# Kernel optimization log

Hardware: AMD Instinct MI355X
Metric: run time of the kernel (lower is better)

Reference implementation:

```python
import jax, jax.numpy as jnp
import numpy as np
from jax.ops import segment_sum

NUM_NODES = 100000
HIDDEN = 128
NUM_LAYERS = 3
EDGES = 640000
BN_EPS = 1e-5


def setup_inputs() -> dict:
    key = jax.random.key(0)
    ks = jax.random.split(key, 6)
    edge_index = jax.random.randint(ks[0], (2, EDGES), 0, NUM_NODES, dtype=jnp.int32)
    # xavier-ish init for embedding (hidden-1 dims; last dim is log-degree feature)
    emb_weight = jax.random.normal(ks[1], (NUM_NODES, HIDDEN - 1), dtype=jnp.float32) * 0.02
    # GCNConv linear weights [L, in, out] and biases [L, out]
    Ws = jax.random.normal(ks[2], (NUM_LAYERS, HIDDEN, HIDDEN), dtype=jnp.float32) * (1.0 / np.sqrt(HIDDEN))
    bs = jnp.zeros((NUM_LAYERS, HIDDEN), dtype=jnp.float32)
    gammas = jnp.ones((NUM_LAYERS, HIDDEN), dtype=jnp.float32)
    betas = jnp.zeros((NUM_LAYERS, HIDDEN), dtype=jnp.float32)
    return {"emb_weight": emb_weight, "Ws": Ws, "bs": bs,
            "gammas": gammas, "betas": betas, "edge_index": edge_index}


def reference(emb_weight, Ws, bs, gammas, betas, edge_index):
    row, col = edge_index[0], edge_index[1]  # source, target
    N = emb_weight.shape[0]
    ones_e = jnp.ones(row.shape[0], dtype=emb_weight.dtype)

    # node_degree_features = log(out_degree + 1) (degree of edge_index[0])
    deg_src = segment_sum(ones_e, row, num_segments=N)
    x = jnp.concatenate([emb_weight, jnp.log(deg_src + 1.0)[:, None]], axis=1)  # [N, H]

    # GCN symmetric normalization (add_self_loops=False): deg over targets
    deg = segment_sum(ones_e, col, num_segments=N)
    dinv = jnp.where(deg > 0, jax.lax.rsqrt(jnp.maximum(deg, 1.0)), 0.0)
    norm = dinv[row] * dinv[col]  # [E]

    for i in range(Ws.shape[0]):
        x_prev = x
        h = x @ Ws[i]  # [N, H]
        # scatter-add of normalized messages: out[col] += norm * h[row]
        agg = segment_sum(norm[:, None] * h[row], col, num_segments=N) + bs[i]
        # BatchNorm1d (batch statistics, biased variance)
        mean = agg.mean(axis=0)
        var = agg.var(axis=0)
        x = gammas[i] * (agg - mean) * jax.lax.rsqrt(var + BN_EPS) + betas[i]
        x = jax.nn.relu(x)
        if i > 0:
            x = x + 0.5 * x_prev
    return x
```

## Files before the change

kernel.cpp:

```cpp
#include <hip/hip_runtime.h>
#include <hip/hip_bf16.h>
#include <math.h>

#define BN_EPS 1e-5f

typedef __attribute__((ext_vector_type(8))) short short8v;
typedef __attribute__((ext_vector_type(4))) float f32x4;

__device__ inline float bf_lo(unsigned int p) { return __uint_as_float(p << 16); }
__device__ inline float bf_hi(unsigned int p) { return __uint_as_float(p & 0xffff0000u); }
__device__ inline unsigned int packbf(float a, float b) {
    unsigned short lo = __builtin_bit_cast(unsigned short, __float2bfloat16(a));
    unsigned short hi = __builtin_bit_cast(unsigned short, __float2bfloat16(b));
    return (unsigned int)lo | ((unsigned int)hi << 16);
}


__global__ __launch_bounds__(256) void deg_kernel(const int* __restrict__ row, const int* __restrict__ col,
                                                  float* __restrict__ deg_src, float* __restrict__ deg_dst, int E) {
    int e = blockIdx.x * 256 + threadIdx.x;
    if (e < E) {
        atomicAdd(&deg_src[row[e]], 1.0f);
        atomicAdd(&deg_dst[col[e]], 1.0f);
    }
}

__global__ __launch_bounds__(256) void dinv_cnt_kernel(float* __restrict__ deg_dst, int* __restrict__ cnt, int N) {
    int n = blockIdx.x * 256 + threadIdx.x;
    if (n < N) {
        float d = deg_dst[n];
        cnt[n] = (int)d;
        deg_dst[n] = (d > 0.0f) ? rsqrtf(d) : 0.0f;
    }
}

__global__ __launch_bounds__(256) void initx_kernel(const float* __restrict__ emb, const float* __restrict__ deg_src,
                                                    unsigned int* __restrict__ x, int N) {
    int idx = blockIdx.x * 256 + threadIdx.x;
    if (idx < N * 64) {
        int n = idx >> 6, p = idx & 63;
        float v0, v1;
        if (p < 63) {
            v0 = emb[(size_t)n * 127 + 2 * p];
            v1 = emb[(size_t)n * 127 + 2 * p + 1];
        } else {
            v0 = emb[(size_t)n * 127 + 126];
            v1 = logf(deg_src[n] + 1.0f);
        }
        x[idx] = packbf(v0, v1);
    }
}

__global__ __launch_bounds__(256) void wt_kernel(const float* __restrict__ Ws, __hip_bfloat16* __restrict__ Wt) {
    int idx = blockIdx.x * 256 + threadIdx.x;
    if (idx < 3 * 16384) {
        int l = idx >> 14, rem = idx & 16383, c = rem >> 7, k = rem & 127;
        Wt[idx] = __float2bfloat16(Ws[(l << 14) + (k << 7) + c]);
    }
}


__global__ __launch_bounds__(256) void scan_pass1(const int* __restrict__ cnt, int* __restrict__ blockSums,
                                                  int N, int PT) {
    __shared__ int lds[256];
    const int tid = threadIdx.x;
    const int start = (blockIdx.x * 256 + tid) * PT;
    int s = 0;
    for (int i = 0; i < PT; ++i) {
        int idx = start + i;
        if (idx < N) s += cnt[idx];
    }
    lds[tid] = s;
    __syncthreads();
    for (int d = 128; d > 0; d >>= 1) {
        if (tid < d) lds[tid] += lds[tid + d];
        __syncthreads();
    }
    if (tid == 0) blockSums[blockIdx.x] = lds[0];
}

__global__ __launch_bounds__(256) void scan_pass2(const int* __restrict__ blockSums, int* __restrict__ blockOffs) {
    __shared__ int lds[256];
    const int tid = threadIdx.x;
    int v = blockSums[tid];
    lds[tid] = v;
    __syncthreads();
    for (int d = 1; d < 256; d <<= 1) {
        int t = (tid >= d) ? lds[tid - d] : 0;
        __syncthreads();
        lds[tid] += t;
        __syncthreads();
    }
    blockOffs[tid] = lds[tid] - v;
}

__global__ __launch_bounds__(256) void scan_pass3(const int* __restrict__ cnt, const int* __restrict__ blockOffs,
                                                  int* __restrict__ off, int* __restrict__ cur,
                                                  int N, int PT, int E) {
    __shared__ int lds[256];
    const int tid = threadIdx.x;
    const int start = (blockIdx.x * 256 + tid) * PT;
    int s = 0;
    for (int i = 0; i < PT; ++i) {
        int idx = start + i;
        if (idx < N) s += cnt[idx];
    }
    lds[tid] = s;
    __syncthreads();
    for (int d = 1; d < 256; d <<= 1) {
        int t = (tid >= d) ? lds[tid - d] : 0;
        __syncthreads();
        lds[tid] += t;
        __syncthreads();
    }
    int prefix = blockOffs[blockIdx.x] + lds[tid] - s;
    for (int i = 0; i < PT; ++i) {
        int idx = start + i;
        if (idx < N) {
            off[idx] = prefix;
            cur[idx] = prefix;
            prefix += cnt[idx];
        }
    }
    if (blockIdx.x == 0 && tid == 0) off[N] = E;
}

__global__ __launch_bounds__(256) void fill_kernel(const int* __restrict__ row, const int* __restrict__ col,
                                                   const float* __restrict__ dinv, int* __restrict__ cur,
                                                   int* __restrict__ srcs, float* __restrict__ wts, int E) {
    int e = blockIdx.x * 256 + threadIdx.x;
    if (e < E) {
        int r = row[e], t = col[e];
        int p = atomicAdd(&cur[t], 1);
        srcs[p] = r;
        wts[p] = dinv[r] * dinv[t];
    }
}


__global__ __launch_bounds__(256) void gemm_mfma(const __hip_bfloat16* __restrict__ X,
                                                 const __hip_bfloat16* __restrict__ Wt,
                                                 __hip_bfloat16* __restrict__ H, int nStripes, int N) {
    const int lane = threadIdx.x & 63;
    const int wv = threadIdx.x >> 6;
    const int r = lane & 15;
    const int q = lane >> 4;
    const int ch = (blockIdx.x * 4 + wv) & 1;

    short8v bfrag[4][4];
#pragma unroll
    for (int ct = 0; ct < 4; ++ct)
#pragma unroll
        for (int kk = 0; kk < 4; ++kk)
            bfrag[ct][kk] = *(const short8v*)(Wt + ((ch * 64 + ct * 16 + r) << 7) + kk * 32 + q * 8);

    const int totalJobs = nStripes * 2;
    for (int job = blockIdx.x * 4 + wv; job < totalJobs; job += gridDim.x * 4) {
        const int s = job >> 1;
        const int arow = s * 16 + r;
        short8v a0 = {}, a1 = {}, a2 = {}, a3 = {};
        if (arow < N) {
            const __hip_bfloat16* xp = X + ((size_t)arow << 7) + q * 8;
            a0 = *(const short8v*)(xp);
            a1 = *(const short8v*)(xp + 32);
            a2 = *(const short8v*)(xp + 64);
            a3 = *(const short8v*)(xp + 96);
        }
        f32x4 acc[4];
#pragma unroll
        for (int ct = 0; ct < 4; ++ct) {
            f32x4 c = {0.f, 0.f, 0.f, 0.f};
            c = __builtin_amdgcn_mfma_f32_16x16x32_bf16(a0, bfrag[ct][0], c, 0, 0, 0);
            c = __builtin_amdgcn_mfma_f32_16x16x32_bf16(a1, bfrag[ct][1], c, 0, 0, 0);
            c = __builtin_amdgcn_mfma_f32_16x16x32_bf16(a2, bfrag[ct][2], c, 0, 0, 0);
            c = __builtin_amdgcn_mfma_f32_16x16x32_bf16(a3, bfrag[ct][3], c, 0, 0, 0);
            acc[ct] = c;
        }
#pragma unroll
        for (int g = 0; g < 4; ++g) {
            int grow = s * 16 + q * 4 + g;
            if (grow < N) {
                __hip_bfloat16* hp = H + ((size_t)grow << 7) + ch * 64 + r;
#pragma unroll
                for (int ct = 0; ct < 4; ++ct)
                    hp[ct * 16] = __float2bfloat16(acc[ct][g]);
            }
        }
    }
}


__global__ __launch_bounds__(256) void gather_kernel(const __hip_bfloat16* __restrict__ h,
                                                     const int* __restrict__ off, const int* __restrict__ srcs,
                                                     const float* __restrict__ wts, const float* __restrict__ bias,
                                                     float* __restrict__ agg, float* __restrict__ sums, int N) {
    __shared__ float sm[2][4][128];
    const int tid = threadIdx.x;
    const int lane = tid & 63;
    const int w = tid >> 6;
    const int g = lane >> 4;
    const int s = lane & 15;

    float b8[8];
    *(float4*)&b8[0] = *(const float4*)&bias[s * 8];
    *(float4*)&b8[4] = *(const float4*)&bias[s * 8 + 4];

    float psum[8], psq[8];
#pragma unroll
    for (int j = 0; j < 8; ++j) { psum[j] = 0.f; psq[j] = 0.f; }

    for (int n0 = blockIdx.x * 4 + w; n0 < N; n0 += gridDim.x * 4) {
        const int n = __builtin_amdgcn_readfirstlane(n0);
        const int sOff = off[n], eOff = off[n + 1];
        float acc[8];
#pragma unroll
        for (int j = 0; j < 8; ++j) acc[j] = 0.f;

        for (int i = sOff; i < eOff; i += 8) {
            int i0 = i + g, i1 = i + 4 + g;
            int idx0 = (i0 < eOff) ? i0 : (eOff - 1);
            int idx1 = (i1 < eOff) ? i1 : (eOff - 1);
            float w0 = (i0 < eOff) ? wts[idx0] : 0.0f;
            float w1 = (i1 < eOff) ? wts[idx1] : 0.0f;
            int r0 = srcs[idx0], r1 = srcs[idx1];
            short8v h0 = *(const short8v*)(h + ((size_t)r0 << 7) + s * 8);
            short8v h1 = *(const short8v*)(h + ((size_t)r1 << 7) + s * 8);
#pragma unroll
            for (int j = 0; j < 4; ++j) {
                unsigned int u0 = ((const unsigned int*)&h0)[j];
                unsigned int u1 = ((const unsigned int*)&h1)[j];
                acc[2 * j]     = fmaf(w0, bf_lo(u0), acc[2 * j]);
                acc[2 * j + 1] = fmaf(w0, bf_hi(u0), acc[2 * j + 1]);
                acc[2 * j]     = fmaf(w1, bf_lo(u1), acc[2 * j]);
                acc[2 * j + 1] = fmaf(w1, bf_hi(u1), acc[2 * j + 1]);
            }
        }
#pragma unroll
        for (int j = 0; j < 8; ++j) {
            acc[j] += __shfl_xor(acc[j], 16);
            acc[j] += __shfl_xor(acc[j], 32);
            acc[j] += b8[j];
        }
        if (g == 0) {
            float* ap = &agg[((size_t)n << 7) + s * 8];
            *(float4*)ap       = make_float4(acc[0], acc[1], acc[2], acc[3]);
            *(float4*)(ap + 4) = make_float4(acc[4], acc[5], acc[6], acc[7]);
#pragma unroll
            for (int j = 0; j < 8; ++j) {
                psum[j] += acc[j];
                psq[j] = fmaf(acc[j], acc[j], psq[j]);
            }
        }
    }
    if (g == 0) {
#pragma unroll
        for (int j = 0; j < 8; ++j) {
            sm[0][w][s * 8 + j] = psum[j];
            sm[1][w][s * 8 + j] = psq[j];
        }
    }
    __syncthreads();
    if (tid < 128) {
        atomicAdd(&sums[tid], sm[0][0][tid] + sm[0][1][tid] + sm[0][2][tid] + sm[0][3][tid]);
    } else {
        int c = tid - 128;
        atomicAdd(&sums[128 + c], sm[1][0][c] + sm[1][1][c] + sm[1][2][c] + sm[1][3][c]);
    }
}


__global__ void bn_finalize(const float* __restrict__ sums, const float* __restrict__ gamma,
                            const float* __restrict__ beta, float* __restrict__ ss, int N) {
    int c = threadIdx.x;
    float mean = sums[c] / (float)N;
    float var  = sums[128 + c] / (float)N - mean * mean;
    float inv  = rsqrtf(fmaxf(var, 0.0f) + BN_EPS);
    float sc   = gamma[c] * inv;
    ss[c]       = sc;
    ss[128 + c] = beta[c] - mean * sc;
}

template <int MODE>
__global__ __launch_bounds__(256) void bn_apply(const float* __restrict__ agg, const float* __restrict__ ss,
                                                const unsigned int* __restrict__ xprev, void* __restrict__ xout,
                                                int NH2) {
    int idx = blockIdx.x * 256 + threadIdx.x;
    if (idx < NH2) {
        int c0 = (idx * 2) & 127;
        float2 v = *(const float2*)&agg[(size_t)idx * 2];
        float r0 = fmaxf(fmaf(v.x, ss[c0],     ss[128 + c0]),     0.0f);
        float r1 = fmaxf(fmaf(v.y, ss[c0 + 1], ss[128 + c0 + 1]), 0.0f);
        if (MODE >= 1) {
            unsigned int xp = xprev[idx];
            r0 = fmaf(0.5f, bf_lo(xp), r0);
            r1 = fmaf(0.5f, bf_hi(xp), r1);
        }
        if (MODE == 2) {
            *(float2*)((float*)xout + (size_t)idx * 2) = make_float2(r0, r1);
        } else {
            ((unsigned int*)xout)[idx] = packbf(r0, r1);
        }
    }
}


extern "C" void kernel_launch(void* const* d_in, const int* in_sizes, int n_in,
                              void* d_out, int out_size, void* d_ws, size_t ws_size,
                              hipStream_t stream) {
    const float* emb    = (const float*)d_in[0];
    const float* Ws     = (const float*)d_in[1];
    const float* bs     = (const float*)d_in[2];
    const float* gammas = (const float*)d_in[3];
    const float* betas  = (const float*)d_in[4];
    const int*   ei     = (const int*)d_in[5];

    const int N = in_sizes[0] / 127;
    const int E = in_sizes[5] / 2;
    const int* row = ei;
    const int* col = ei + E;
    float* out = (float*)d_out;

    const size_t NH = (size_t)N * 128;
    __hip_bfloat16* XA = (__hip_bfloat16*)d_ws;
    __hip_bfloat16* XB = XA + NH;
    __hip_bfloat16* Wt = XB + NH;
    float* deg_src = (float*)(Wt + 3 * 16384);
    float* dinvb   = deg_src + N;
    float* wts     = dinvb + N;
    float* sums    = wts + E;
    float* ssb     = sums + 256;
    int*   cnt     = (int*)(ssb + 256);
    int*   cur     = cnt + N;
    int*   srcs    = cur + N;
    int*   blockSums = srcs + E;
    int*   blockOffs = blockSums + 256;
    int*   off     = blockOffs + 256;
    float* agg     = out;

    const int NH2 = (int)(NH / 2);
    const int PT = (N + 65535) / 65536;
    const int nStripes = (N + 15) / 16;

    hipMemsetAsync(deg_src, 0, sizeof(float) * 2 * (size_t)N, stream);
    wt_kernel<<<(3 * 16384 + 255) / 256, 256, 0, stream>>>(Ws, Wt);
    deg_kernel<<<(E + 255) / 256, 256, 0, stream>>>(row, col, deg_src, dinvb, E);
    dinv_cnt_kernel<<<(N + 255) / 256, 256, 0, stream>>>(dinvb, cnt, N);
    initx_kernel<<<(N * 64 + 255) / 256, 256, 0, stream>>>(emb, deg_src, (unsigned int*)XA, N);
    scan_pass1<<<256, 256, 0, stream>>>(cnt, blockSums, N, PT);
    scan_pass2<<<1, 256, 0, stream>>>(blockSums, blockOffs);
    scan_pass3<<<256, 256, 0, stream>>>(cnt, blockOffs, off, cur, N, PT, E);
    fill_kernel<<<(E + 255) / 256, 256, 0, stream>>>(row, col, dinvb, cur, srcs, wts, E);

    const __hip_bfloat16* xin[3]  = {XA, XA, XB};
    __hip_bfloat16*       hbuf[3] = {XB, XB, XA};

    for (int i = 0; i < 3; ++i) {
        gemm_mfma<<<1024, 256, 0, stream>>>(xin[i], Wt + (size_t)i * 16384, hbuf[i], nStripes, N);
        hipMemsetAsync(sums, 0, sizeof(float) * 256, stream);
        gather_kernel<<<2048, 256, 0, stream>>>(hbuf[i], off, srcs, wts, bs + i * 128, agg, sums, N);
        bn_finalize<<<1, 128, 0, stream>>>(sums, gammas + i * 128, betas + i * 128, ssb, N);
        if (i == 0)
            bn_apply<0><<<(NH2 + 255) / 256, 256, 0, stream>>>(agg, ssb, (const unsigned int*)xin[i], (void*)XA, NH2);
        else if (i == 1)
            bn_apply<1><<<(NH2 + 255) / 256, 256, 0, stream>>>(agg, ssb, (const unsigned int*)xin[i], (void*)XB, NH2);
        else
            bn_apply<2><<<(NH2 + 255) / 256, 256, 0, stream>>>(agg, ssb, (const unsigned int*)xin[i], (void*)out, NH2);
    }
}
```

Measured before the change: 495.5 us.

## Pack edge metadata, store bf16 aggregates, process two nodes per wave, fold BN finalize

Source index and weight now sit together in one int2 array, so the gather issues a single load per edge. Each wave now handles two consecutive nodes at once to raise memory-level parallelism. The aggregate buffer is written as bf16 instead of fp32, which halves its traffic. The sums memset moves into the GEMM kernel and the BN finalize step is folded into bn_apply, which removes launches. The cost is bf16 rounding of pre-BN aggregates, which hurts precision, plus per-thread recomputation of BN scale and shift.

```diff
diff --git a/kernel.cpp b/kernel.cpp
--- a/kernel.cpp
+++ b/kernel.cpp
@@ -127,20 +127,22 @@
 
 __global__ __launch_bounds__(256) void fill_kernel(const int* __restrict__ row, const int* __restrict__ col,
                                                    const float* __restrict__ dinv, int* __restrict__ cur,
-                                                   int* __restrict__ srcs, float* __restrict__ wts, int E) {
+                                                   int2* __restrict__ meta, int E) {
     int e = blockIdx.x * 256 + threadIdx.x;
     if (e < E) {
         int r = row[e], t = col[e];
         int p = atomicAdd(&cur[t], 1);
-        srcs[p] = r;
-        wts[p] = dinv[r] * dinv[t];
+        meta[p] = make_int2(r, __float_as_int(dinv[r] * dinv[t]));
     }
 }
 
 
 __global__ __launch_bounds__(256) void gemm_mfma(const __hip_bfloat16* __restrict__ X,
                                                  const __hip_bfloat16* __restrict__ Wt,
-                                                 __hip_bfloat16* __restrict__ H, int nStripes, int N) {
+                                                 __hip_bfloat16* __restrict__ H, float* __restrict__ sums,
+                                                 int nStripes, int N) {
+    if (blockIdx.x == 0) sums[threadIdx.x] = 0.0f;
+
     const int lane = threadIdx.x & 63;
     const int wv = threadIdx.x >> 6;
     const int r = lane & 15;
@@ -191,9 +193,9 @@
 
 
 __global__ __launch_bounds__(256) void gather_kernel(const __hip_bfloat16* __restrict__ h,
-                                                     const int* __restrict__ off, const int* __restrict__ srcs,
-                                                     const float* __restrict__ wts, const float* __restrict__ bias,
-                                                     float* __restrict__ agg, float* __restrict__ sums, int N) {
+                                                     const int* __restrict__ off, const int2* __restrict__ meta,
+                                                     const float* __restrict__ bias,
+                                                     unsigned int* __restrict__ aggb, float* __restrict__ sums, int N) {
     __shared__ float sm[2][4][128];
     const int tid = threadIdx.x;
     const int lane = tid & 63;
@@ -209,47 +211,84 @@
 #pragma unroll
     for (int j = 0; j < 8; ++j) { psum[j] = 0.f; psq[j] = 0.f; }
 
-    for (int n0 = blockIdx.x * 4 + w; n0 < N; n0 += gridDim.x * 4) {
-        const int n = __builtin_amdgcn_readfirstlane(n0);
-        const int sOff = off[n], eOff = off[n + 1];
-        float acc[8];
-#pragma unroll
-        for (int j = 0; j < 8; ++j) acc[j] = 0.f;
-
-        for (int i = sOff; i < eOff; i += 8) {
-            int i0 = i + g, i1 = i + 4 + g;
-            int idx0 = (i0 < eOff) ? i0 : (eOff - 1);
-            int idx1 = (i1 < eOff) ? i1 : (eOff - 1);
-            float w0 = (i0 < eOff) ? wts[idx0] : 0.0f;
-            float w1 = (i1 < eOff) ? wts[idx1] : 0.0f;
-            int r0 = srcs[idx0], r1 = srcs[idx1];
-            short8v h0 = *(const short8v*)(h + ((size_t)r0 << 7) + s * 8);
-            short8v h1 = *(const short8v*)(h + ((size_t)r1 << 7) + s * 8);
+    for (int base = (blockIdx.x * 4 + w) * 2; base < N; base += gridDim.x * 8) {
+        const int nA = __builtin_amdgcn_readfirstlane(base);
+        const int hasB = (nA + 1 < N);
+        const int sA = off[nA];
+        const int eA = off[nA + 1];
+        const int eB = hasB ? off[nA + 2] : eA;
+
+        float accA[8], accB[8];
+#pragma unroll
+        for (int j = 0; j < 8; ++j) { accA[j] = 0.f; accB[j] = 0.f; }
+
+        int iA = sA, iB = eA;
+        while (iA < eA || iB < eB) {
+            int i0A = iA + g, i1A = iA + 4 + g;
+            int i0B = iB + g, i1B = iB + 4 + g;
+            int idx0A = (i0A < eA) ? i0A : 0;
+            int idx1A = (i1A < eA) ? i1A : 0;
+            int idx0B = (i0B < eB) ? i0B : 0;
+            int idx1B = (i1B < eB) ? i1B : 0;
+            int2 m0A = meta[idx0A], m1A = meta[idx1A];
+            int2 m0B = meta[idx0B], m1B = meta[idx1B];
+            float w0A = (i0A < eA) ? __int_as_float(m0A.y) : 0.f;
+            float w1A = (i1A < eA) ? __int_as_float(m1A.y) : 0.f;
+            float w0B = (i0B < eB) ? __int_as_float(m0B.y) : 0.f;
+            float w1B = (i1B < eB) ? __int_as_float(m1B.y) : 0.f;
+            short8v h0A = *(const short8v*)(h + ((size_t)m0A.x << 7) + s * 8);
+            short8v h1A = *(const short8v*)(h + ((size_t)m1A.x << 7) + s * 8);
+            short8v h0B = *(const short8v*)(h + ((size_t)m0B.x << 7) + s * 8);
+            short8v h1B = *(const short8v*)(h + ((size_t)m1B.x << 7) + s * 8);
 #pragma unroll
             for (int j = 0; j < 4; ++j) {
-                unsigned int u0 = ((const unsigned int*)&h0)[j];
-                unsigned int u1 = ((const unsigned int*)&h1)[j];
-                acc[2 * j]     = fmaf(w0, bf_lo(u0), acc[2 * j]);
-                acc[2 * j + 1] = fmaf(w0, bf_hi(u0), acc[2 * j + 1]);
-                acc[2 * j]     = fmaf(w1, bf_lo(u1), acc[2 * j]);
-                acc[2 * j + 1] = fmaf(w1, bf_hi(u1), acc[2 * j + 1]);
+                unsigned int u;
+                u = ((const unsigned int*)&h0A)[j];
+                accA[2 * j]     = fmaf(w0A, bf_lo(u), accA[2 * j]);
+                accA[2 * j + 1] = fmaf(w0A, bf_hi(u), accA[2 * j + 1]);
+                u = ((const unsigned int*)&h1A)[j];
+                accA[2 * j]     = fmaf(w1A, bf_lo(u), accA[2 * j]);
+                accA[2 * j + 1] = fmaf(w1A, bf_hi(u), accA[2 * j + 1]);
+                u = ((const unsigned int*)&h0B)[j];
+                accB[2 * j]     = fmaf(w0B, bf_lo(u), accB[2 * j]);
+                accB[2 * j + 1] = fmaf(w0B, bf_hi(u), accB[2 * j + 1]);
+                u = ((const unsigned int*)&h1B)[j];
+                accB[2 * j]     = fmaf(w1B, bf_lo(u), accB[2 * j]);
+                accB[2 * j + 1] = fmaf(w1B, bf_hi(u), accB[2 * j + 1]);
             }
+            iA += 8; iB += 8;
         }
 #pragma unroll
         for (int j = 0; j < 8; ++j) {
-            acc[j] += __shfl_xor(acc[j], 16);
-            acc[j] += __shfl_xor(acc[j], 32);
-            acc[j] += b8[j];
+            accA[j] += __shfl_xor(accA[j], 16);
+            accA[j] += __shfl_xor(accA[j], 32);
+            accA[j] += b8[j];
+            accB[j] += __shfl_xor(accB[j], 16);
+            accB[j] += __shfl_xor(accB[j], 32);
+            accB[j] += b8[j];
         }
         if (g == 0) {
-            float* ap = &agg[((size_t)n << 7) + s * 8];
-            *(float4*)ap       = make_float4(acc[0], acc[1], acc[2], acc[3]);
-            *(float4*)(ap + 4) = make_float4(acc[4], acc[5], acc[6], acc[7]);
+            unsigned int pk[4];
+#pragma unroll
+            for (int j = 0; j < 4; ++j) pk[j] = packbf(accA[2 * j], accA[2 * j + 1]);
+            *(uint4*)(aggb + ((size_t)nA << 6) + s * 4) = *(uint4*)pk;
 #pragma unroll
             for (int j = 0; j < 8; ++j) {
-                psum[j] += acc[j];
-                psq[j] = fmaf(acc[j], acc[j], psq[j]);
+                psum[j] += accA[j];
+                psq[j] = fmaf(accA[j], accA[j], psq[j]);
             }
+            if (hasB) {
+#pragma unroll
+                for (int j = 0; j < 8; ++j) {
+                    psum[j] += accB[j];
+                    psq[j] = fmaf(accB[j], accB[j], psq[j]);
+                }
+            }
+        } else if (g == 1 && hasB) {
+            unsigned int pk[4];
+#pragma unroll
+            for (int j = 0; j < 4; ++j) pk[j] = packbf(accB[2 * j], accB[2 * j + 1]);
+            *(uint4*)(aggb + ((size_t)(nA + 1) << 6) + s * 4) = *(uint4*)pk;
         }
     }
     if (g == 0) {
@@ -269,37 +308,61 @@
 }
 
 
-__global__ void bn_finalize(const float* __restrict__ sums, const float* __restrict__ gamma,
-                            const float* __restrict__ beta, float* __restrict__ ss, int N) {
-    int c = threadIdx.x;
-    float mean = sums[c] / (float)N;
-    float var  = sums[128 + c] / (float)N - mean * mean;
-    float inv  = rsqrtf(fmaxf(var, 0.0f) + BN_EPS);
-    float sc   = gamma[c] * inv;
-    ss[c]       = sc;
-    ss[128 + c] = beta[c] - mean * sc;
-}
-
 template <int MODE>
-__global__ __launch_bounds__(256) void bn_apply(const float* __restrict__ agg, const float* __restrict__ ss,
-                                                const unsigned int* __restrict__ xprev, void* __restrict__ xout,
-                                                int NH2) {
+__global__ __launch_bounds__(256) void bn_apply(const uint4* __restrict__ aggb, const float* __restrict__ sums,
+                                                const float* __restrict__ gamma, const float* __restrict__ beta,
+                                                const uint4* __restrict__ xprev, void* __restrict__ xout,
+                                                int NO, float invN) {
     int idx = blockIdx.x * 256 + threadIdx.x;
-    if (idx < NH2) {
-        int c0 = (idx * 2) & 127;
-        float2 v = *(const float2*)&agg[(size_t)idx * 2];
-        float r0 = fmaxf(fmaf(v.x, ss[c0],     ss[128 + c0]),     0.0f);
-        float r1 = fmaxf(fmaf(v.y, ss[c0 + 1], ss[128 + c0 + 1]), 0.0f);
-        if (MODE >= 1) {
-            unsigned int xp = xprev[idx];
-            r0 = fmaf(0.5f, bf_lo(xp), r0);
-            r1 = fmaf(0.5f, bf_hi(xp), r1);
-        }
-        if (MODE == 2) {
-            *(float2*)((float*)xout + (size_t)idx * 2) = make_float2(r0, r1);
-        } else {
-            ((unsigned int*)xout)[idx] = packbf(r0, r1);
-        }
+    if (idx >= NO) return;
+    const int c0 = (idx & 15) * 8;
+
+    float su[8], sq[8], gm[8], bt[8];
+    *(float4*)&su[0] = *(const float4*)&sums[c0];
+    *(float4*)&su[4] = *(const float4*)&sums[c0 + 4];
+    *(float4*)&sq[0] = *(const float4*)&sums[128 + c0];
+    *(float4*)&sq[4] = *(const float4*)&sums[128 + c0 + 4];
+    *(float4*)&gm[0] = *(const float4*)&gamma[c0];
+    *(float4*)&gm[4] = *(const float4*)&gamma[c0 + 4];
+    *(float4*)&bt[0] = *(const float4*)&beta[c0];
+    *(float4*)&bt[4] = *(const float4*)&beta[c0 + 4];
+
+    float sc[8], sh[8];
+#pragma unroll
+    for (int j = 0; j < 8; ++j) {
+        float m = su[j] * invN;
+        float v = sq[j] * invN - m * m;
+        float inv = rsqrtf(fmaxf(v, 0.0f) + BN_EPS);
+        sc[j] = gm[j] * inv;
+        sh[j] = bt[j] - m * sc[j];
+    }
+
+    uint4 av = aggb[idx];
+    const unsigned int* au = (const unsigned int*)&av;
+    float r[8];
+#pragma unroll
+    for (int j = 0; j < 4; ++j) {
+        r[2 * j]     = fmaxf(fmaf(bf_lo(au[j]), sc[2 * j],     sh[2 * j]),     0.f);
+        r[2 * j + 1] = fmaxf(fmaf(bf_hi(au[j]), sc[2 * j + 1], sh[2 * j + 1]), 0.f);
+    }
+    if (MODE >= 1) {
+        uint4 xv = xprev[idx];
+        const unsigned int* xu = (const unsigned int*)&xv;
+#pragma unroll
+        for (int j = 0; j < 4; ++j) {
+            r[2 * j]     = fmaf(0.5f, bf_lo(xu[j]), r[2 * j]);
+            r[2 * j + 1] = fmaf(0.5f, bf_hi(xu[j]), r[2 * j + 1]);
+        }
+    }
+    if (MODE == 2) {
+        float* op = (float*)xout + (size_t)idx * 8;
+        *(float4*)op       = make_float4(r[0], r[1], r[2], r[3]);
+        *(float4*)(op + 4) = make_float4(r[4], r[5], r[6], r[7]);
+    } else {
+        unsigned int pk[4];
+#pragma unroll
+        for (int j = 0; j < 4; ++j) pk[j] = packbf(r[2 * j], r[2 * j + 1]);
+        ((uint4*)xout)[idx] = *(uint4*)pk;
     }
 }
 
@@ -323,23 +386,22 @@
     const size_t NH = (size_t)N * 128;
     __hip_bfloat16* XA = (__hip_bfloat16*)d_ws;
     __hip_bfloat16* XB = XA + NH;
-    __hip_bfloat16* Wt = XB + NH;
+    unsigned int*  AGG = (unsigned int*)(XB + NH);
+    int2*         meta = (int2*)(AGG + NH / 2);
+    __hip_bfloat16* Wt = (__hip_bfloat16*)(meta + E);
     float* deg_src = (float*)(Wt + 3 * 16384);
     float* dinvb   = deg_src + N;
-    float* wts     = dinvb + N;
-    float* sums    = wts + E;
-    float* ssb     = sums + 256;
-    int*   cnt     = (int*)(ssb + 256);
+    float* sums    = dinvb + N;
+    int*   cnt     = (int*)(sums + 256);
     int*   cur     = cnt + N;
-    int*   srcs    = cur + N;
-    int*   blockSums = srcs + E;
+    int*   blockSums = cur + N;
     int*   blockOffs = blockSums + 256;
     int*   off     = blockOffs + 256;
-    float* agg     = out;
-
-    const int NH2 = (int)(NH / 2);
+
+    const int NO = (int)(NH / 8);
     const int PT = (N + 65535) / 65536;
     const int nStripes = (N + 15) / 16;
+    const float invN = 1.0f / (float)N;
 
     hipMemsetAsync(deg_src, 0, sizeof(float) * 2 * (size_t)N, stream);
     wt_kernel<<<(3 * 16384 + 255) / 256, 256, 0, stream>>>(Ws, Wt);
@@ -349,21 +411,22 @@
     scan_pass1<<<256, 256, 0, stream>>>(cnt, blockSums, N, PT);
     scan_pass2<<<1, 256, 0, stream>>>(blockSums, blockOffs);
     scan_pass3<<<256, 256, 0, stream>>>(cnt, blockOffs, off, cur, N, PT, E);
-    fill_kernel<<<(E + 255) / 256, 256, 0, stream>>>(row, col, dinvb, cur, srcs, wts, E);
+    fill_kernel<<<(E + 255) / 256, 256, 0, stream>>>(row, col, dinvb, cur, meta, E);
 
     const __hip_bfloat16* xin[3]  = {XA, XA, XB};
     __hip_bfloat16*       hbuf[3] = {XB, XB, XA};
 
     for (int i = 0; i < 3; ++i) {
-        gemm_mfma<<<1024, 256, 0, stream>>>(xin[i], Wt + (size_t)i * 16384, hbuf[i], nStripes, N);
-        hipMemsetAsync(sums, 0, sizeof(float) * 256, stream);
-        gather_kernel<<<2048, 256, 0, stream>>>(hbuf[i], off, srcs, wts, bs + i * 128, agg, sums, N);
-        bn_finalize<<<1, 128, 0, stream>>>(sums, gammas + i * 128, betas + i * 128, ssb, N);
+        gemm_mfma<<<1024, 256, 0, stream>>>(xin[i], Wt + (size_t)i * 16384, hbuf[i], sums, nStripes, N);
+        gather_kernel<<<2048, 256, 0, stream>>>(hbuf[i], off, meta, bs + i * 128, AGG, sums, N);
         if (i == 0)
-            bn_apply<0><<<(NH2 + 255) / 256, 256, 0, stream>>>(agg, ssb, (const unsigned int*)xin[i], (void*)XA, NH2);
+            bn_apply<0><<<(NO + 255) / 256, 256, 0, stream>>>((const uint4*)AGG, sums, gammas, betas,
+                                                              (const uint4*)xin[i], (void*)XA, NO, invN);
         else if (i == 1)
-            bn_apply<1><<<(NH2 + 255) / 256, 256, 0, stream>>>(agg, ssb, (const unsigned int*)xin[i], (void*)XB, NH2);
+            bn_apply<1><<<(NO + 255) / 256, 256, 0, stream>>>((const uint4*)AGG, sums, gammas + 128, betas + 128,
+                                                              (const uint4*)xin[i], (void*)XB, NO, invN);
         else
-            bn_apply<2><<<(NH2 + 255) / 256, 256, 0, stream>>>(agg, ssb, (const unsigned int*)xin[i], (void*)out, NH2);
-    }
-}
+            bn_apply<2><<<(NO + 255) / 256, 256, 0, stream>>>((const uint4*)AGG, sums, gammas + 256, betas + 256,
+                                                              (const uint4*)xin[i], (void*)out, NO, invN);
+    }
+}
```

Result: faster. 445.7 us (-10.0%).
